# Performance work log

Measured on AMD Instinct MI355X. Metric: run time of the kernel, lower is better.

Reference implementation:

```python
import jax, jax.numpy as jnp
import numpy as np

B, S, D_IN = 2, 2048, 1024
EMBED, HEADS = 1024, 16
HEAD_DIM = EMBED // HEADS

def setup_inputs() -> dict:
    key = jax.random.key(0)
    k1, k2, k3 = jax.random.split(key, 3)
    # xavier_uniform bounds
    def xavier(k, shape):
        fan_in, fan_out = shape[1], shape[0]
        lim = jnp.sqrt(6.0 / (fan_in + fan_out))
        return jax.random.uniform(k, shape, jnp.float32, -lim, lim)
    x = jax.random.normal(k1, (B, S, D_IN), jnp.float32)
    qkv_w = xavier(k2, (3 * EMBED, D_IN))   # torch Linear weight layout [out, in]
    qkv_b = jnp.zeros((3 * EMBED,), jnp.float32)
    o_w = xavier(k3, (EMBED, EMBED))
    o_b = jnp.zeros((EMBED,), jnp.float32)
    return {"x": x, "qkv_w": qkv_w, "qkv_b": qkv_b, "o_w": o_w, "o_b": o_b}

def reference(x, qkv_w, qkv_b, o_w, o_b):
    Bq, Sq, _ = x.shape
    qkv = x @ qkv_w.T + qkv_b                       # [B,S,3E]
    qkv = qkv.reshape(Bq, Sq, HEADS, 3 * HEAD_DIM).transpose(0, 2, 1, 3)  # [B,H,S,3d]
    q, k, v = jnp.split(qkv, 3, axis=-1)            # each [B,H,S,d]
    scale = 1.0 / jnp.sqrt(jnp.asarray(HEAD_DIM, x.dtype))
    logits = jnp.einsum('bhqd,bhkd->bhqk', q, k) * scale
    attn = jax.nn.softmax(logits, axis=-1)
    vals = jnp.einsum('bhqk,bhkd->bhqd', attn, v)   # [B,H,S,d]
    vals = vals.transpose(0, 2, 1, 3).reshape(Bq, Sq, EMBED)
    return vals @ o_w.T + o_b
```

## Files before the change

### kernel.cpp

```cpp
#include <hip/hip_runtime.h>
#include <hip/hip_bf16.h>

#define B_    2
#define S_    2048
#define DIN   1024
#define EMB   1024
#define NH    16
#define HD    64
#define N3    3072
#define MROWS 4096
#define KVB   64
#define QBLK  128
#define NT    (S_ / KVB)

typedef short bf16x8 __attribute__((ext_vector_type(8)));
typedef float f32x4  __attribute__((ext_vector_type(4)));
typedef float f32x16 __attribute__((ext_vector_type(16)));
typedef unsigned short u16;
typedef u16 u16x8 __attribute__((ext_vector_type(8)));
typedef u16 u16x4 __attribute__((ext_vector_type(4)));
typedef unsigned int u32;

__device__ __forceinline__ u16 f2bf(float f) {
  union { float f; unsigned u; } x; x.f = f;
  unsigned r = x.u + 0x7fffu + ((x.u >> 16) & 1u);
  return (u16)(r >> 16);
}

__device__ __forceinline__ u32 cvtpk(float lo, float hi) {
  u32 r;
  asm("v_cvt_pk_bf16_f32 %0, %1, %2" : "=v"(r) : "v"(lo), "v"(hi));
  return r;
}

__device__ __forceinline__ void gload16(const void* g, void* l) {
  __builtin_amdgcn_global_load_lds(
      (const __attribute__((address_space(1))) unsigned int*)g,
      (__attribute__((address_space(3))) unsigned int*)l, 16, 0, 0);
}

__global__ void cast4(const float* __restrict__ in, u16* __restrict__ out, int n4) {
  const int i = blockIdx.x * 256 + threadIdx.x;
  if (i < n4) {
    const float4 v = ((const float4*)in)[i];
    u16x4 o;
    o[0] = f2bf(v.x); o[1] = f2bf(v.y); o[2] = f2bf(v.z); o[3] = f2bf(v.w);
    ((u16x4*)out)[i] = o;
  }
}

template<int EPI>
__global__ __launch_bounds__(256)
void gemm_bt(const u16* __restrict__ A, const u16* __restrict__ W,
             const float* __restrict__ bias, float* __restrict__ Cf,
             u16* __restrict__ Qb, u16* __restrict__ Kb, u16* __restrict__ VbT,
             int M, int N, int K) {
  __shared__ u16 Als[128 * 32];
  __shared__ u16 Bls[128 * 32];
  const int tid  = threadIdx.x;
  const int wave = tid >> 6, lane = tid & 63;
  const int lhi  = lane >> 4, llo = lane & 15;
  const int wr   = wave >> 1, wc = wave & 1;
  const int m0   = blockIdx.y * 128, n0 = blockIdx.x * 128;

  const f32x4 fzero = {0.f, 0.f, 0.f, 0.f};
  f32x4 acc[4][4];
#pragma unroll
  for (int m = 0; m < 4; ++m)
#pragma unroll
    for (int n = 0; n < 4; ++n) acc[m][n] = fzero;

  for (int k0 = 0; k0 < K; k0 += 32) {
#pragma unroll
    for (int i = 0; i < 2; ++i) {
      const int e   = (tid + i * 256) * 8;
      const int row = e >> 5, col = e & 31;
      gload16(A + (size_t)(m0 + row) * K + k0 + col, (char*)Als + wave * 1024 + i * 4096);
      gload16(W + (size_t)(n0 + row) * K + k0 + col, (char*)Bls + wave * 1024 + i * 4096);
    }
    __syncthreads();
    bf16x8 af[4], bfr[4];
#pragma unroll
    for (int m = 0; m < 4; ++m) af[m]  = *(const bf16x8*)&Als[(wr * 64 + m * 16 + llo) * 32 + lhi * 8];
#pragma unroll
    for (int n = 0; n < 4; ++n) bfr[n] = *(const bf16x8*)&Bls[(wc * 64 + n * 16 + llo) * 32 + lhi * 8];
#pragma unroll
    for (int m = 0; m < 4; ++m)
#pragma unroll
      for (int n = 0; n < 4; ++n)
        acc[m][n] = __builtin_amdgcn_mfma_f32_16x16x32_bf16(af[m], bfr[n], acc[m][n], 0, 0, 0);
    __syncthreads();
  }

#pragma unroll
  for (int n = 0; n < 4; ++n) {
    const int colb = n0 + wc * 64 + n * 16;
    const int gcol = colb + llo;
    const float bv = bias[gcol];
    if (EPI == 0) {
      const int h   = colb / 192;
      const int rr  = colb - h * 192;
      const int sec = rr >> 6;
      const int d   = (rr & 63) + llo;
#pragma unroll
      for (int m = 0; m < 4; ++m) {
        const int rowb = m0 + wr * 64 + m * 16 + lhi * 4;
        const int b = rowb >> 11, s0 = rowb & 2047;
        if (sec == 2) {
          u16x4 vv;
#pragma unroll
          for (int r = 0; r < 4; ++r) vv[r] = f2bf(acc[m][n][r] + bv);
          *(u16x4*)&VbT[((size_t)(b * NH + h) * HD + d) * S_ + s0] = vv;
        } else {
          u16* dst = (sec == 0) ? Qb : Kb;
          const float scl = (sec == 0) ? 0.18033688f : 1.0f;
#pragma unroll
          for (int r = 0; r < 4; ++r)
            dst[(((size_t)(b * NH + h) * S_ + s0 + r) << 6) + d] = f2bf((acc[m][n][r] + bv) * scl);
        }
      }
    } else {
#pragma unroll
      for (int m = 0; m < 4; ++m) {
        const int rowb = m0 + wr * 64 + m * 16 + lhi * 4;
#pragma unroll
        for (int r = 0; r < 4; ++r)
          Cf[(size_t)(rowb + r) * N + gcol] = acc[m][n][r] + bv;
      }
    }
  }
}

__global__ __launch_bounds__(256)
void attn_fwd(const u16* __restrict__ Qb, const u16* __restrict__ Kb,
              const u16* __restrict__ VbT, u16* __restrict__ Obf) {
  __shared__ __align__(16) u16 Kls[4][KVB * HD];
  __shared__ __align__(16) u16 Vls[4][HD * KVB];
  __shared__ __align__(16) float sBc[4][32];
  const int tid  = threadIdx.x;
  const int wave = tid >> 6, lane = tid & 63;
  const int q    = lane & 31, hi = lane >> 5;
  const int bh   = blockIdx.y;
  const int q0   = blockIdx.x * QBLK;
  const size_t base  = (size_t)bh * S_ * HD;
  const size_t basev = (size_t)bh * HD * S_;

  const int qrow = q0 + wave * 32 + q;
  bf16x8 qf[4];
#pragma unroll
  for (int c = 0; c < 4; ++c)
    qf[c] = *(const bf16x8*)&Qb[base + (size_t)qrow * HD + c * 16 + hi * 8];

  const int srow = tid >> 3;
  const int xs   = (tid & 7) ^ (srow & 7);
  const u16* kSrc = Kb  + base  + (size_t)srow * HD + xs * 8;
  const u16* vSrc = VbT + basev + (size_t)srow * S_ + xs * 8;
  const int ldsW = wave * 1024;

  const int gq = 16 * (q >> 4) + 8 * ((q >> 2) & 1) + (q & 3) + 4 * ((q >> 3) & 1);

  int offK[2][4], offV[2][4];
#pragma unroll
  for (int b = 0; b < 2; ++b)
#pragma unroll
    for (int c = 0; c < 4; ++c) {
      offK[b][c] = (b * 32 + gq) * 128 + (((c * 2 + hi) ^ (gq & 7)) << 4);
      offV[b][c] = (b * 32 + q)  * 128 + (((c * 2 + hi) ^ (q  & 7)) << 4);
    }

  f32x16 o0, o1;
#pragma unroll
  for (int r = 0; r < 16; ++r) { o0[r] = 0.f; o1[r] = 0.f; }
  float m_run = -1e30f, lsum = 0.f;

  auto issue = [&](int t) {
#pragma unroll
    for (int p = 0; p < 2; ++p) {
      gload16(kSrc + (size_t)t * KVB * HD + (size_t)p * 32 * HD,
              (char*)Kls[t & 3] + p * 4096 + ldsW);
      gload16(vSrc + t * KVB + (size_t)p * 32 * S_,
              (char*)Vls[t & 3] + p * 4096 + ldsW);
    }
  };

  auto compute = [&](int t) {
    const char* Kt = (const char*)Kls[t & 3];
    const char* Vt = (const char*)Vls[t & 3];

    f32x16 s0, s1;
#pragma unroll
    for (int r = 0; r < 16; ++r) { s0[r] = 0.f; s1[r] = 0.f; }
    __builtin_amdgcn_s_setprio(1);
#pragma unroll
    for (int c = 0; c < 4; ++c) {
      bf16x8 k0 = *(const bf16x8*)(Kt + offK[0][c]);
      bf16x8 k1 = *(const bf16x8*)(Kt + offK[1][c]);
      s0 = __builtin_amdgcn_mfma_f32_32x32x16_bf16(k0, qf[c], s0, 0, 0, 0);
      s1 = __builtin_amdgcn_mfma_f32_32x32x16_bf16(k1, qf[c], s1, 0, 0, 0);
    }
    __builtin_amdgcn_s_setprio(0);

    float tm[16];
#pragma unroll
    for (int r = 0; r < 16; ++r) tm[r] = fmaxf(s0[r], s1[r]);
#pragma unroll
    for (int st = 8; st >= 1; st >>= 1)
#pragma unroll
      for (int i = 0; i < 16; ++i) if (i < st) tm[i] = fmaxf(tm[i], tm[i + st]);
    const float pm = fmaxf(tm[0], __shfl_xor(tm[0], 32));

    if (__any(pm > m_run + 10.0f)) {
      const float mnew  = fmaxf(m_run, pm);
      const float alpha = exp2f(m_run - mnew);
      sBc[wave][q] = alpha;
      asm volatile("s_waitcnt lgkmcnt(0)" ::: "memory");
      f32x4 av[4];
#pragma unroll
      for (int g = 0; g < 4; ++g) av[g] = *(const f32x4*)&sBc[wave][hi * 4 + g * 8];
#pragma unroll
      for (int r = 0; r < 16; ++r) {
        const float f = av[r >> 2][r & 3];
        o0[r] *= f; o1[r] *= f;
      }
      lsum *= alpha;
      m_run = mnew;
    }

    float t0 = 0.f, t1 = 0.f, t2 = 0.f, t3 = 0.f;
    u32 dw0[8], dw1[8];
#pragma unroll
    for (int j = 0; j < 8; ++j) {
      const float a0 = exp2f(s0[2 * j] - m_run), a1 = exp2f(s0[2 * j + 1] - m_run);
      const float b0 = exp2f(s1[2 * j] - m_run), b1 = exp2f(s1[2 * j + 1] - m_run);
      t0 += a0; t1 += a1; t2 += b0; t3 += b1;
      dw0[j] = cvtpk(a0, a1);
      dw1[j] = cvtpk(b0, b1);
    }
    float ts = (t0 + t1) + (t2 + t3);
    ts += __shfl_xor(ts, 32);
    lsum += ts;

    __builtin_amdgcn_s_setprio(1);
#pragma unroll
    for (int c = 0; c < 4; ++c) {
      union { u32 u[4]; bf16x8 v; } P;
      if (c == 0)      { P.u[0] = dw0[0]; P.u[1] = dw0[1]; P.u[2] = dw0[2]; P.u[3] = dw0[3]; }
      else if (c == 1) { P.u[0] = dw0[4]; P.u[1] = dw0[5]; P.u[2] = dw0[6]; P.u[3] = dw0[7]; }
      else if (c == 2) { P.u[0] = dw1[0]; P.u[1] = dw1[1]; P.u[2] = dw1[2]; P.u[3] = dw1[3]; }
      else             { P.u[0] = dw1[4]; P.u[1] = dw1[5]; P.u[2] = dw1[6]; P.u[3] = dw1[7]; }
      bf16x8 v0 = *(const bf16x8*)(Vt + offV[0][c]);
      bf16x8 v1 = *(const bf16x8*)(Vt + offV[1][c]);
      o0 = __builtin_amdgcn_mfma_f32_32x32x16_bf16(P.v, v0, o0, 0, 0, 0);
      o1 = __builtin_amdgcn_mfma_f32_32x32x16_bf16(P.v, v1, o1, 0, 0, 0);
    }
    __builtin_amdgcn_s_setprio(0);
  };

  issue(0); issue(1);

#define BAR() do { asm volatile("" ::: "memory"); \
                   __builtin_amdgcn_s_barrier();  \
                   asm volatile("" ::: "memory"); } while (0)
  for (int p = 0; p < NT / 2 - 1; ++p) {
    issue(2 * p + 2); issue(2 * p + 3);
    asm volatile("s_waitcnt vmcnt(8)" ::: "memory");
    BAR();
    compute(2 * p);
    compute(2 * p + 1);
    BAR();
  }
  asm volatile("s_waitcnt vmcnt(0)" ::: "memory");
  BAR();
  compute(NT - 2);
  compute(NT - 1);
#undef BAR

  const float li = 1.0f / lsum;
  sBc[wave][q] = li;
  asm volatile("s_waitcnt lgkmcnt(0)" ::: "memory");
  f32x4 lv[4];
#pragma unroll
  for (int g = 0; g < 4; ++g) lv[g] = *(const f32x4*)&sBc[wave][hi * 4 + g * 8];
  const int b = bh >> 4, h = bh & 15;
#pragma unroll
  for (int r = 0; r < 16; ++r) {
    const int qg = q0 + wave * 32 + (r & 3) + 8 * (r >> 2) + 4 * hi;
    const float f = lv[r >> 2][r & 3];
    u16* dst = Obf + ((size_t)(b * S_ + qg) * NH + h) * HD;
    dst[q]      = f2bf(o0[r] * f);
    dst[32 + q] = f2bf(o1[r] * f);
  }
}

extern "C" void kernel_launch(void* const* d_in, const int* in_sizes, int n_in,
                              void* d_out, int out_size, void* d_ws, size_t ws_size,
                              hipStream_t stream) {
  const float* x     = (const float*)d_in[0];
  const float* qkv_w = (const float*)d_in[1];
  const float* qkv_b = (const float*)d_in[2];
  const float* o_w   = (const float*)d_in[3];
  const float* o_b   = (const float*)d_in[4];
  float* out = (float*)d_out;

  char* ws = (char*)d_ws;
  u16* xbf  = (u16*)(ws);
  u16* wqkv = (u16*)(ws + (8u  << 20));
  u16* wo   = (u16*)(ws + (14u << 20));
  u16* Qb   = (u16*)(ws + (16u << 20));
  u16* Kb   = (u16*)(ws + (24u << 20));
  u16* VbT  = (u16*)(ws + (32u << 20));
  u16* atnb = xbf;

  cast4<<<4096, 256, 0, stream>>>(x,     xbf,  1048576);
  cast4<<<3072, 256, 0, stream>>>(qkv_w, wqkv,  786432);
  cast4<<<1024, 256, 0, stream>>>(o_w,   wo,    262144);

  gemm_bt<0><<<dim3(N3 / 128, MROWS / 128), 256, 0, stream>>>(
      xbf, wqkv, qkv_b, nullptr, Qb, Kb, VbT, MROWS, N3, DIN);

  attn_fwd<<<dim3(S_ / QBLK, B_ * NH), 256, 0, stream>>>(Qb, Kb, VbT, atnb);

  gemm_bt<1><<<dim3(EMB / 128, MROWS / 128), 256, 0, stream>>>(
      atnb, wo, o_b, out, nullptr, nullptr, nullptr, MROWS, EMB, EMB);
}
```

Baseline: 151.7 us.

## Split attention over KV halves with combine pass, fuse cast kernels

Attention now splits the KV sequence into two halves across a third grid dimension. Each half writes fp32 partial outputs plus running max and sum, and a separate combine kernel merges them into bf16. This doubles the block count from 512 to 1024 so the GPU's CUs stay busier, at the cost of extra fp32 traffic (about 32 MB written and read) and one more launch. The three cast kernels are also merged into one launch. The split path only runs when the workspace is large enough, otherwise the old kernel is used.

```diff
diff --git a/kernel.cpp b/kernel.cpp
--- a/kernel.cpp
+++ b/kernel.cpp
@@ -12,6 +12,8 @@
 #define KVB   64
 #define QBLK  128
 #define NT    (S_ / KVB)
+#define NSPL  2
+#define NTS   (NT / NSPL)
 
 typedef short bf16x8 __attribute__((ext_vector_type(8)));
 typedef float f32x4  __attribute__((ext_vector_type(4)));
@@ -39,14 +41,19 @@
       (__attribute__((address_space(3))) unsigned int*)l, 16, 0, 0);
 }
 
-__global__ void cast4(const float* __restrict__ in, u16* __restrict__ out, int n4) {
+__global__ __launch_bounds__(256)
+void cast_all(const float* __restrict__ x, const float* __restrict__ w1,
+              const float* __restrict__ w2, u16* __restrict__ ox,
+              u16* __restrict__ ow1, u16* __restrict__ ow2) {
   const int i = blockIdx.x * 256 + threadIdx.x;
-  if (i < n4) {
-    const float4 v = ((const float4*)in)[i];
-    u16x4 o;
-    o[0] = f2bf(v.x); o[1] = f2bf(v.y); o[2] = f2bf(v.z); o[3] = f2bf(v.w);
-    ((u16x4*)out)[i] = o;
-  }
+  const float* src; u16* dst; int off;
+  if (i < 1048576)              { src = x;  dst = ox;  off = i; }
+  else if (i < 1048576 + 786432){ src = w1; dst = ow1; off = i - 1048576; }
+  else                          { src = w2; dst = ow2; off = i - 1835008; }
+  const float4 v = ((const float4*)src)[off];
+  u16x4 o;
+  o[0] = f2bf(v.x); o[1] = f2bf(v.y); o[2] = f2bf(v.z); o[3] = f2bf(v.w);
+  ((u16x4*)dst)[off] = o;
 }
 
 template<int EPI>
@@ -131,6 +138,182 @@
   }
 }
 
+
+__global__ __launch_bounds__(256)
+void attn_split(const u16* __restrict__ Qb, const u16* __restrict__ Kb,
+                const u16* __restrict__ VbT, float* __restrict__ Op,
+                float2* __restrict__ Ml) {
+  __shared__ __align__(16) u16 Kls[2][KVB * HD];
+  __shared__ __align__(16) u16 Vls[2][HD * KVB];
+  __shared__ __align__(16) float sBc[4][32];
+  const int tid  = threadIdx.x;
+  const int wave = tid >> 6, lane = tid & 63;
+  const int q    = lane & 31, hi = lane >> 5;
+  const int bh   = blockIdx.y;
+  const int q0   = blockIdx.x * QBLK;
+  const int sp   = blockIdx.z;
+  const size_t base  = (size_t)bh * S_ * HD;
+  const size_t basev = (size_t)bh * HD * S_;
+
+  const int qrow = q0 + wave * 32 + q;
+  bf16x8 qf[4];
+#pragma unroll
+  for (int c = 0; c < 4; ++c)
+    qf[c] = *(const bf16x8*)&Qb[base + (size_t)qrow * HD + c * 16 + hi * 8];
+
+  const int srow = tid >> 3;
+  const int xs   = (tid & 7) ^ (srow & 7);
+  const u16* kSrc = Kb  + base  + (size_t)(sp * NTS * KVB + srow) * HD + xs * 8;
+  const u16* vSrc = VbT + basev + (size_t)srow * S_ + sp * NTS * KVB + xs * 8;
+  const int ldsW = wave * 1024;
+
+  const int gq = 16 * (q >> 4) + 8 * ((q >> 2) & 1) + (q & 3) + 4 * ((q >> 3) & 1);
+  int offK[2][4], offV[2][4];
+#pragma unroll
+  for (int b = 0; b < 2; ++b)
+#pragma unroll
+    for (int c = 0; c < 4; ++c) {
+      offK[b][c] = (b * 32 + gq) * 128 + (((c * 2 + hi) ^ (gq & 7)) << 4);
+      offV[b][c] = (b * 32 + q)  * 128 + (((c * 2 + hi) ^ (q  & 7)) << 4);
+    }
+
+  f32x16 o0, o1;
+#pragma unroll
+  for (int r = 0; r < 16; ++r) { o0[r] = 0.f; o1[r] = 0.f; }
+  float m_run = -1e30f, lsum = 0.f;
+
+  auto issue = [&](int t) {
+#pragma unroll
+    for (int p = 0; p < 2; ++p) {
+      gload16(kSrc + (size_t)t * KVB * HD + (size_t)p * 32 * HD,
+              (char*)Kls[t & 1] + p * 4096 + ldsW);
+      gload16(vSrc + t * KVB + (size_t)p * 32 * S_,
+              (char*)Vls[t & 1] + p * 4096 + ldsW);
+    }
+  };
+
+  auto compute = [&](int t) {
+    const char* Kt = (const char*)Kls[t & 1];
+    const char* Vt = (const char*)Vls[t & 1];
+
+    f32x16 s0, s1;
+#pragma unroll
+    for (int r = 0; r < 16; ++r) { s0[r] = 0.f; s1[r] = 0.f; }
+    __builtin_amdgcn_s_setprio(1);
+#pragma unroll
+    for (int c = 0; c < 4; ++c) {
+      bf16x8 k0 = *(const bf16x8*)(Kt + offK[0][c]);
+      bf16x8 k1 = *(const bf16x8*)(Kt + offK[1][c]);
+      s0 = __builtin_amdgcn_mfma_f32_32x32x16_bf16(k0, qf[c], s0, 0, 0, 0);
+      s1 = __builtin_amdgcn_mfma_f32_32x32x16_bf16(k1, qf[c], s1, 0, 0, 0);
+    }
+    __builtin_amdgcn_s_setprio(0);
+
+    float tm[16];
+#pragma unroll
+    for (int r = 0; r < 16; ++r) tm[r] = fmaxf(s0[r], s1[r]);
+#pragma unroll
+    for (int st = 8; st >= 1; st >>= 1)
+#pragma unroll
+      for (int i = 0; i < 16; ++i) if (i < st) tm[i] = fmaxf(tm[i], tm[i + st]);
+    const float pm = fmaxf(tm[0], __shfl_xor(tm[0], 32));
+
+    if (__any(pm > m_run + 10.0f)) {
+      const float mnew  = fmaxf(m_run, pm);
+      const float alpha = exp2f(m_run - mnew);
+      sBc[wave][q] = alpha;
+      asm volatile("s_waitcnt lgkmcnt(0)" ::: "memory");
+      f32x4 av[4];
+#pragma unroll
+      for (int g = 0; g < 4; ++g) av[g] = *(const f32x4*)&sBc[wave][hi * 4 + g * 8];
+#pragma unroll
+      for (int r = 0; r < 16; ++r) {
+        const float f = av[r >> 2][r & 3];
+        o0[r] *= f; o1[r] *= f;
+      }
+      lsum *= alpha;
+      m_run = mnew;
+    }
+
+    float t0 = 0.f, t1 = 0.f, t2 = 0.f, t3 = 0.f;
+    u32 dw0[8], dw1[8];
+#pragma unroll
+    for (int j = 0; j < 8; ++j) {
+      const float a0 = exp2f(s0[2 * j] - m_run), a1 = exp2f(s0[2 * j + 1] - m_run);
+      const float b0 = exp2f(s1[2 * j] - m_run), b1 = exp2f(s1[2 * j + 1] - m_run);
+      t0 += a0; t1 += a1; t2 += b0; t3 += b1;
+      dw0[j] = cvtpk(a0, a1);
+      dw1[j] = cvtpk(b0, b1);
+    }
+    float ts = (t0 + t1) + (t2 + t3);
+    ts += __shfl_xor(ts, 32);
+    lsum += ts;
+
+    __builtin_amdgcn_s_setprio(1);
+#pragma unroll
+    for (int c = 0; c < 4; ++c) {
+      union { u32 u[4]; bf16x8 v; } P;
+      if (c == 0)      { P.u[0] = dw0[0]; P.u[1] = dw0[1]; P.u[2] = dw0[2]; P.u[3] = dw0[3]; }
+      else if (c == 1) { P.u[0] = dw0[4]; P.u[1] = dw0[5]; P.u[2] = dw0[6]; P.u[3] = dw0[7]; }
+      else if (c == 2) { P.u[0] = dw1[0]; P.u[1] = dw1[1]; P.u[2] = dw1[2]; P.u[3] = dw1[3]; }
+      else             { P.u[0] = dw1[4]; P.u[1] = dw1[5]; P.u[2] = dw1[6]; P.u[3] = dw1[7]; }
+      bf16x8 v0 = *(const bf16x8*)(Vt + offV[0][c]);
+      bf16x8 v1 = *(const bf16x8*)(Vt + offV[1][c]);
+      o0 = __builtin_amdgcn_mfma_f32_32x32x16_bf16(P.v, v0, o0, 0, 0, 0);
+      o1 = __builtin_amdgcn_mfma_f32_32x32x16_bf16(P.v, v1, o1, 0, 0, 0);
+    }
+    __builtin_amdgcn_s_setprio(0);
+  };
+
+#define BAR() do { asm volatile("" ::: "memory"); \
+                   __builtin_amdgcn_s_barrier();  \
+                   asm volatile("" ::: "memory"); } while (0)
+  issue(0);
+  for (int t = 0; t < NTS - 1; ++t) {
+    issue(t + 1);
+    asm volatile("s_waitcnt vmcnt(4)" ::: "memory");
+    BAR();
+    compute(t);
+    BAR();
+  }
+  asm volatile("s_waitcnt vmcnt(0)" ::: "memory");
+  BAR();
+  compute(NTS - 1);
+#undef BAR
+
+  float* dstb = Op + (size_t)(sp * (B_ * NH) + bh) * S_ * HD;
+#pragma unroll
+  for (int r = 0; r < 16; ++r) {
+    const int qg = q0 + wave * 32 + (r & 3) + 8 * (r >> 2) + 4 * hi;
+    float* dst = dstb + (size_t)qg * HD;
+    dst[q]      = o0[r];
+    dst[32 + q] = o1[r];
+  }
+  if (hi == 0)
+    Ml[(size_t)(sp * (B_ * NH) + bh) * S_ + qrow] = make_float2(m_run, lsum);
+}
+
+__global__ __launch_bounds__(256)
+void attn_combine(const float* __restrict__ Op, const float2* __restrict__ Ml,
+                  u16* __restrict__ atnb) {
+  const int g  = blockIdx.x * 256 + threadIdx.x;
+  const int d4 = g & 15, q = (g >> 4) & (S_ - 1), bh = g >> 15;
+  const float2 ml0 = Ml[(size_t)bh * S_ + q];
+  const float2 ml1 = Ml[(size_t)(B_ * NH + bh) * S_ + q];
+  const float M  = fmaxf(ml0.x, ml1.x);
+  const float w0 = exp2f(ml0.x - M), w1 = exp2f(ml1.x - M);
+  const float inv = 1.0f / (w0 * ml0.y + w1 * ml1.y);
+  const float4 a = ((const float4*)(Op + ((size_t)bh * S_ + q) * HD))[d4];
+  const float4 b = ((const float4*)(Op + ((size_t)(B_ * NH + bh) * S_ + q) * HD))[d4];
+  const int bb = bh >> 4, h = bh & 15;
+  u16x4 o;
+  o[0] = f2bf((w0 * a.x + w1 * b.x) * inv);
+  o[1] = f2bf((w0 * a.y + w1 * b.y) * inv);
+  o[2] = f2bf((w0 * a.z + w1 * b.z) * inv);
+  o[3] = f2bf((w0 * a.w + w1 * b.w) * inv);
+  ((u16x4*)(atnb + ((size_t)(bb * S_ + q) * NH + h) * HD))[d4] = o;
+}
+
 __global__ __launch_bounds__(256)
 void attn_fwd(const u16* __restrict__ Qb, const u16* __restrict__ Kb,
               const u16* __restrict__ VbT, u16* __restrict__ Obf) {
@@ -158,7 +341,6 @@
   const int ldsW = wave * 1024;
 
   const int gq = 16 * (q >> 4) + 8 * ((q >> 2) & 1) + (q & 3) + 4 * ((q >> 3) & 1);
-
   int offK[2][4], offV[2][4];
 #pragma unroll
   for (int b = 0; b < 2; ++b)
@@ -186,7 +368,6 @@
   auto compute = [&](int t) {
     const char* Kt = (const char*)Kls[t & 3];
     const char* Vt = (const char*)Vls[t & 3];
-
     f32x16 s0, s1;
 #pragma unroll
     for (int r = 0; r < 16; ++r) { s0[r] = 0.f; s1[r] = 0.f; }
@@ -257,7 +438,6 @@
   };
 
   issue(0); issue(1);
-
 #define BAR() do { asm volatile("" ::: "memory"); \
                    __builtin_amdgcn_s_barrier();  \
                    asm volatile("" ::: "memory"); } while (0)
@@ -311,14 +491,23 @@
   u16* VbT  = (u16*)(ws + (32u << 20));
   u16* atnb = xbf;
 
-  cast4<<<4096, 256, 0, stream>>>(x,     xbf,  1048576);
-  cast4<<<3072, 256, 0, stream>>>(qkv_w, wqkv,  786432);
-  cast4<<<1024, 256, 0, stream>>>(o_w,   wo,    262144);
+  const size_t opBytes = (size_t)NSPL * B_ * NH * S_ * HD * sizeof(float);
+  const size_t mlBytes = (size_t)NSPL * B_ * NH * S_ * sizeof(float2);
+  const size_t NEED = ((size_t)40 << 20) + opBytes + mlBytes;
+  float*  Op = (float*)(ws + ((size_t)40 << 20));
+  float2* Ml = (float2*)(ws + ((size_t)40 << 20) + opBytes);
+
+  cast_all<<<8192, 256, 0, stream>>>(x, qkv_w, o_w, xbf, wqkv, wo);
 
   gemm_bt<0><<<dim3(N3 / 128, MROWS / 128), 256, 0, stream>>>(
       xbf, wqkv, qkv_b, nullptr, Qb, Kb, VbT, MROWS, N3, DIN);
 
-  attn_fwd<<<dim3(S_ / QBLK, B_ * NH), 256, 0, stream>>>(Qb, Kb, VbT, atnb);
+  if (ws_size >= NEED) {
+    attn_split<<<dim3(S_ / QBLK, B_ * NH, NSPL), 256, 0, stream>>>(Qb, Kb, VbT, Op, Ml);
+    attn_combine<<<(B_ * NH * S_ * HD / 4) / 256, 256, 0, stream>>>(Op, Ml, atnb);
+  } else {
+    attn_fwd<<<dim3(S_ / QBLK, B_ * NH), 256, 0, stream>>>(Qb, Kb, VbT, atnb);
+  }
 
   gemm_bt<1><<<dim3(EMB / 128, MROWS / 128), 256, 0, stream>>>(
       atnb, wo, o_b, out, nullptr, nullptr, nullptr, MROWS, EMB, EMB);
```

Measured after the change: 155.8 us. +2.7%, slower.

## Add triple-buffered 256x128 QKV GEMM kernel and merge cast launches

Applied to the files above, without the earlier changes.

Replaces the generic 128x128 QKV projection GEMM with a dedicated 512-thread kernel. It uses 256x128 tiles, K-steps of 64, triple-buffered async global-to-LDS loads with an XOR-swizzled layout, and a block-index swizzle for L2 locality. The three fp32-to-bf16 cast launches are merged into one kernel to cut launch overhead. The larger tile raises LDS use (about 144 KB), which allows one block per CU and only 384 blocks, so wave-count balance across CUs may suffer.

```diff
diff --git a/kernel.cpp b/kernel.cpp
--- a/kernel.cpp
+++ b/kernel.cpp
@@ -39,22 +39,142 @@
       (__attribute__((address_space(3))) unsigned int*)l, 16, 0, 0);
 }
 
-__global__ void cast4(const float* __restrict__ in, u16* __restrict__ out, int n4) {
+#define BARRIER() do { asm volatile("" ::: "memory"); \
+                       __builtin_amdgcn_s_barrier();  \
+                       asm volatile("" ::: "memory"); } while (0)
+
+__global__ __launch_bounds__(256)
+void cast_all(const float* __restrict__ x, const float* __restrict__ w1,
+              const float* __restrict__ w2, u16* __restrict__ ox,
+              u16* __restrict__ ow1, u16* __restrict__ ow2) {
   const int i = blockIdx.x * 256 + threadIdx.x;
-  if (i < n4) {
-    const float4 v = ((const float4*)in)[i];
-    u16x4 o;
-    o[0] = f2bf(v.x); o[1] = f2bf(v.y); o[2] = f2bf(v.z); o[3] = f2bf(v.w);
-    ((u16x4*)out)[i] = o;
-  }
-}
-
-template<int EPI>
+  const float* src; u16* dst; int off;
+  if (i < 1048576)              { src = x;  dst = ox;  off = i; }
+  else if (i < 1048576 + 786432){ src = w1; dst = ow1; off = i - 1048576; }
+  else                          { src = w2; dst = ow2; off = i - 1835008; }
+  const float4 v = ((const float4*)src)[off];
+  u16x4 o;
+  o[0] = f2bf(v.x); o[1] = f2bf(v.y); o[2] = f2bf(v.z); o[3] = f2bf(v.w);
+  ((u16x4*)dst)[off] = o;
+}
+
+__global__ __launch_bounds__(512)
+void gemm256_qkv(const u16* __restrict__ A, const u16* __restrict__ W,
+                 const float* __restrict__ bias,
+                 u16* __restrict__ Qb, u16* __restrict__ Kb, u16* __restrict__ VbT) {
+  __shared__ __align__(16) u16 Als[3][256 * 64];
+  __shared__ __align__(16) u16 Bls[3][128 * 64];
+  const int K = DIN, KT = DIN / 64;
+
+  const int flat = blockIdx.x;
+  const int swz  = (flat & 7) * 48 + (flat >> 3);
+  const int n0   = (swz % 24) * 128;
+  const int m0   = (swz / 24) * 256;
+
+  const int tid  = threadIdx.x;
+  const int wave = tid >> 6, lane = tid & 63;
+  const int lhi  = lane >> 4, llo = lane & 15;
+  const int wr   = wave >> 2;
+  const int wc   = wave & 3;
+  const int ldsW = wave * 1024;
+
+  const int srow = tid >> 3;
+  const int xcol = (tid & 7) ^ (srow & 7);
+  const u16* aSrc = A + (size_t)(m0 + srow) * K + xcol * 8;
+  const u16* bSrc = W + (size_t)(n0 + srow) * K + xcol * 8;
+
+  auto issue = [&](int t) {
+    const int buf = t % 3;
+#pragma unroll
+    for (int g = 0; g < 4; ++g)
+      gload16(aSrc + (size_t)(g * 64) * K + t * 64,
+              (char*)Als[buf] + g * 8192 + ldsW);
+#pragma unroll
+    for (int g = 0; g < 2; ++g)
+      gload16(bSrc + (size_t)(g * 64) * K + t * 64,
+              (char*)Bls[buf] + g * 8192 + ldsW);
+  };
+
+  int swzs[2];
+#pragma unroll
+  for (int kk = 0; kk < 2; ++kk)
+    swzs[kk] = (((kk * 4 + lhi) ^ (llo & 7)) << 4);
+
+  f32x4 acc[8][2];
+#pragma unroll
+  for (int m = 0; m < 8; ++m)
+#pragma unroll
+    for (int n = 0; n < 2; ++n) acc[m][n] = f32x4{0.f, 0.f, 0.f, 0.f};
+
+  auto compute = [&](int t) {
+    const char* bufA = (const char*)Als[t % 3];
+    const char* bufB = (const char*)Bls[t % 3];
+    bf16x8 bF[2][2];
+#pragma unroll
+    for (int nj = 0; nj < 2; ++nj)
+#pragma unroll
+      for (int kk = 0; kk < 2; ++kk)
+        bF[nj][kk] = *(const bf16x8*)(bufB + (wc * 32 + nj * 16 + llo) * 128 + swzs[kk]);
+    __builtin_amdgcn_s_setprio(1);
+#pragma unroll
+    for (int mi = 0; mi < 8; ++mi) {
+      const char* ap = bufA + (wr * 128 + mi * 16 + llo) * 128;
+      bf16x8 a0 = *(const bf16x8*)(ap + swzs[0]);
+      bf16x8 a1 = *(const bf16x8*)(ap + swzs[1]);
+      acc[mi][0] = __builtin_amdgcn_mfma_f32_16x16x32_bf16(a0, bF[0][0], acc[mi][0], 0, 0, 0);
+      acc[mi][0] = __builtin_amdgcn_mfma_f32_16x16x32_bf16(a1, bF[0][1], acc[mi][0], 0, 0, 0);
+      acc[mi][1] = __builtin_amdgcn_mfma_f32_16x16x32_bf16(a0, bF[1][0], acc[mi][1], 0, 0, 0);
+      acc[mi][1] = __builtin_amdgcn_mfma_f32_16x16x32_bf16(a1, bF[1][1], acc[mi][1], 0, 0, 0);
+    }
+    __builtin_amdgcn_s_setprio(0);
+  };
+
+  issue(0); issue(1);
+  for (int t = 0; t < KT - 2; ++t) {
+    issue(t + 2);
+    asm volatile("s_waitcnt vmcnt(12)" ::: "memory");
+    BARRIER();
+    compute(t);
+    BARRIER();
+  }
+  asm volatile("s_waitcnt vmcnt(6)" ::: "memory");
+  BARRIER(); compute(KT - 2); BARRIER();
+  asm volatile("s_waitcnt vmcnt(0)" ::: "memory");
+  BARRIER(); compute(KT - 1);
+
+#pragma unroll
+  for (int nj = 0; nj < 2; ++nj) {
+    const int colb = n0 + wc * 32 + nj * 16;
+    const int gcol = colb + llo;
+    const float bv = bias[gcol];
+    const int h   = colb / 192;
+    const int rr  = colb - h * 192;
+    const int sec = rr >> 6;
+    const int d   = (rr & 63) + llo;
+#pragma unroll
+    for (int mi = 0; mi < 8; ++mi) {
+      const int rowb = m0 + wr * 128 + mi * 16 + lhi * 4;
+      const int b = rowb >> 11, s0 = rowb & 2047;
+      if (sec == 2) {
+        u16x4 vv;
+#pragma unroll
+        for (int r = 0; r < 4; ++r) vv[r] = f2bf(acc[mi][nj][r] + bv);
+        *(u16x4*)&VbT[((size_t)(b * NH + h) * HD + d) * S_ + s0] = vv;
+      } else {
+        u16* dst = (sec == 0) ? Qb : Kb;
+        const float scl = (sec == 0) ? 0.18033688f : 1.0f;
+#pragma unroll
+        for (int r = 0; r < 4; ++r)
+          dst[(((size_t)(b * NH + h) * S_ + s0 + r) << 6) + d] = f2bf((acc[mi][nj][r] + bv) * scl);
+      }
+    }
+  }
+}
+
 __global__ __launch_bounds__(256)
-void gemm_bt(const u16* __restrict__ A, const u16* __restrict__ W,
-             const float* __restrict__ bias, float* __restrict__ Cf,
-             u16* __restrict__ Qb, u16* __restrict__ Kb, u16* __restrict__ VbT,
-             int M, int N, int K) {
+void gemm_bt_f32(const u16* __restrict__ A, const u16* __restrict__ W,
+                 const float* __restrict__ bias, float* __restrict__ Cf,
+                 int M, int N, int K) {
   __shared__ u16 Als[128 * 32];
   __shared__ u16 Bls[128 * 32];
   const int tid  = threadIdx.x;
@@ -63,12 +183,11 @@
   const int wr   = wave >> 1, wc = wave & 1;
   const int m0   = blockIdx.y * 128, n0 = blockIdx.x * 128;
 
-  const f32x4 fzero = {0.f, 0.f, 0.f, 0.f};
   f32x4 acc[4][4];
 #pragma unroll
   for (int m = 0; m < 4; ++m)
 #pragma unroll
-    for (int n = 0; n < 4; ++n) acc[m][n] = fzero;
+    for (int n = 0; n < 4; ++n) acc[m][n] = f32x4{0.f, 0.f, 0.f, 0.f};
 
   for (int k0 = 0; k0 < K; k0 += 32) {
 #pragma unroll
@@ -94,39 +213,14 @@
 
 #pragma unroll
   for (int n = 0; n < 4; ++n) {
-    const int colb = n0 + wc * 64 + n * 16;
-    const int gcol = colb + llo;
+    const int gcol = n0 + wc * 64 + n * 16 + llo;
     const float bv = bias[gcol];
-    if (EPI == 0) {
-      const int h   = colb / 192;
-      const int rr  = colb - h * 192;
-      const int sec = rr >> 6;
-      const int d   = (rr & 63) + llo;
-#pragma unroll
-      for (int m = 0; m < 4; ++m) {
-        const int rowb = m0 + wr * 64 + m * 16 + lhi * 4;
-        const int b = rowb >> 11, s0 = rowb & 2047;
-        if (sec == 2) {
-          u16x4 vv;
-#pragma unroll
-          for (int r = 0; r < 4; ++r) vv[r] = f2bf(acc[m][n][r] + bv);
-          *(u16x4*)&VbT[((size_t)(b * NH + h) * HD + d) * S_ + s0] = vv;
-        } else {
-          u16* dst = (sec == 0) ? Qb : Kb;
-          const float scl = (sec == 0) ? 0.18033688f : 1.0f;
-#pragma unroll
-          for (int r = 0; r < 4; ++r)
-            dst[(((size_t)(b * NH + h) * S_ + s0 + r) << 6) + d] = f2bf((acc[m][n][r] + bv) * scl);
-        }
-      }
-    } else {
-#pragma unroll
-      for (int m = 0; m < 4; ++m) {
-        const int rowb = m0 + wr * 64 + m * 16 + lhi * 4;
-#pragma unroll
-        for (int r = 0; r < 4; ++r)
-          Cf[(size_t)(rowb + r) * N + gcol] = acc[m][n][r] + bv;
-      }
+#pragma unroll
+    for (int m = 0; m < 4; ++m) {
+      const int rowb = m0 + wr * 64 + m * 16 + lhi * 4;
+#pragma unroll
+      for (int r = 0; r < 4; ++r)
+        Cf[(size_t)(rowb + r) * N + gcol] = acc[m][n][r] + bv;
     }
   }
 }
@@ -158,7 +252,6 @@
   const int ldsW = wave * 1024;
 
   const int gq = 16 * (q >> 4) + 8 * ((q >> 2) & 1) + (q & 3) + 4 * ((q >> 3) & 1);
-
   int offK[2][4], offV[2][4];
 #pragma unroll
   for (int b = 0; b < 2; ++b)
@@ -186,7 +279,6 @@
   auto compute = [&](int t) {
     const char* Kt = (const char*)Kls[t & 3];
     const char* Vt = (const char*)Vls[t & 3];
-
     f32x16 s0, s1;
 #pragma unroll
     for (int r = 0; r < 16; ++r) { s0[r] = 0.f; s1[r] = 0.f; }
@@ -257,23 +349,18 @@
   };
 
   issue(0); issue(1);
-
-#define BAR() do { asm volatile("" ::: "memory"); \
-                   __builtin_amdgcn_s_barrier();  \
-                   asm volatile("" ::: "memory"); } while (0)
   for (int p = 0; p < NT / 2 - 1; ++p) {
     issue(2 * p + 2); issue(2 * p + 3);
     asm volatile("s_waitcnt vmcnt(8)" ::: "memory");
-    BAR();
+    BARRIER();
     compute(2 * p);
     compute(2 * p + 1);
-    BAR();
+    BARRIER();
   }
   asm volatile("s_waitcnt vmcnt(0)" ::: "memory");
-  BAR();
+  BARRIER();
   compute(NT - 2);
   compute(NT - 1);
-#undef BAR
 
   const float li = 1.0f / lsum;
   sBc[wave][q] = li;
@@ -311,15 +398,12 @@
   u16* VbT  = (u16*)(ws + (32u << 20));
   u16* atnb = xbf;
 
-  cast4<<<4096, 256, 0, stream>>>(x,     xbf,  1048576);
-  cast4<<<3072, 256, 0, stream>>>(qkv_w, wqkv,  786432);
-  cast4<<<1024, 256, 0, stream>>>(o_w,   wo,    262144);
-
-  gemm_bt<0><<<dim3(N3 / 128, MROWS / 128), 256, 0, stream>>>(
-      xbf, wqkv, qkv_b, nullptr, Qb, Kb, VbT, MROWS, N3, DIN);
+  cast_all<<<8192, 256, 0, stream>>>(x, qkv_w, o_w, xbf, wqkv, wo);
+
+  gemm256_qkv<<<384, 512, 0, stream>>>(xbf, wqkv, qkv_b, Qb, Kb, VbT);
 
   attn_fwd<<<dim3(S_ / QBLK, B_ * NH), 256, 0, stream>>>(Qb, Kb, VbT, atnb);
 
-  gemm_bt<1><<<dim3(EMB / 128, MROWS / 128), 256, 0, stream>>>(
-      atnb, wo, o_b, out, nullptr, nullptr, nullptr, MROWS, EMB, EMB);
-}
+  gemm_bt_f32<<<dim3(EMB / 128, MROWS / 128), 256, 0, stream>>>(
+      atnb, wo, o_b, out, MROWS, EMB, EMB);
+}
```

Result: slower. 160.1 us (+5.5%).

## Interleave QK and softmax/PV stages across tile pairs in attention loop

Applied to the files above, without the earlier changes.

The per-tile compute lambda is split into separate QK, softmax and PV stages. Both QK products of a tile pair are issued before the first softmax, so the tensor-core work of the second tile can overlap the exponentials of the first. The s_setprio hints are removed and the attention kernel gets launch_bounds(256,2) to cap registers for two blocks per CU. Holding the extra score and packed-P registers raises register pressure, and the new cap may force spills.

```diff
diff --git a/kernel.cpp b/kernel.cpp
--- a/kernel.cpp
+++ b/kernel.cpp
@@ -38,6 +38,10 @@
       (const __attribute__((address_space(1))) unsigned int*)g,
       (__attribute__((address_space(3))) unsigned int*)l, 16, 0, 0);
 }
+
+#define BARRIER() do { asm volatile("" ::: "memory"); \
+                       __builtin_amdgcn_s_barrier();  \
+                       asm volatile("" ::: "memory"); } while (0)
 
 __global__ void cast4(const float* __restrict__ in, u16* __restrict__ out, int n4) {
   const int i = blockIdx.x * 256 + threadIdx.x;
@@ -63,12 +67,11 @@
   const int wr   = wave >> 1, wc = wave & 1;
   const int m0   = blockIdx.y * 128, n0 = blockIdx.x * 128;
 
-  const f32x4 fzero = {0.f, 0.f, 0.f, 0.f};
   f32x4 acc[4][4];
 #pragma unroll
   for (int m = 0; m < 4; ++m)
 #pragma unroll
-    for (int n = 0; n < 4; ++n) acc[m][n] = fzero;
+    for (int n = 0; n < 4; ++n) acc[m][n] = f32x4{0.f, 0.f, 0.f, 0.f};
 
   for (int k0 = 0; k0 < K; k0 += 32) {
 #pragma unroll
@@ -131,7 +134,7 @@
   }
 }
 
-__global__ __launch_bounds__(256)
+__global__ __launch_bounds__(256, 2)
 void attn_fwd(const u16* __restrict__ Qb, const u16* __restrict__ Kb,
               const u16* __restrict__ VbT, u16* __restrict__ Obf) {
   __shared__ __align__(16) u16 Kls[4][KVB * HD];
@@ -158,7 +161,6 @@
   const int ldsW = wave * 1024;
 
   const int gq = 16 * (q >> 4) + 8 * ((q >> 2) & 1) + (q & 3) + 4 * ((q >> 3) & 1);
-
   int offK[2][4], offV[2][4];
 #pragma unroll
   for (int b = 0; b < 2; ++b)
@@ -183,14 +185,10 @@
     }
   };
 
-  auto compute = [&](int t) {
+  auto qk = [&](int t, f32x16& s0, f32x16& s1) {
     const char* Kt = (const char*)Kls[t & 3];
-    const char* Vt = (const char*)Vls[t & 3];
-
-    f32x16 s0, s1;
 #pragma unroll
     for (int r = 0; r < 16; ++r) { s0[r] = 0.f; s1[r] = 0.f; }
-    __builtin_amdgcn_s_setprio(1);
 #pragma unroll
     for (int c = 0; c < 4; ++c) {
       bf16x8 k0 = *(const bf16x8*)(Kt + offK[0][c]);
@@ -198,8 +196,9 @@
       s0 = __builtin_amdgcn_mfma_f32_32x32x16_bf16(k0, qf[c], s0, 0, 0, 0);
       s1 = __builtin_amdgcn_mfma_f32_32x32x16_bf16(k1, qf[c], s1, 0, 0, 0);
     }
-    __builtin_amdgcn_s_setprio(0);
-
+  };
+
+  auto sm = [&](f32x16& s0, f32x16& s1, u32 (&dw0)[8], u32 (&dw1)[8]) {
     float tm[16];
 #pragma unroll
     for (int r = 0; r < 16; ++r) tm[r] = fmaxf(s0[r], s1[r]);
@@ -227,7 +226,6 @@
     }
 
     float t0 = 0.f, t1 = 0.f, t2 = 0.f, t3 = 0.f;
-    u32 dw0[8], dw1[8];
 #pragma unroll
     for (int j = 0; j < 8; ++j) {
       const float a0 = exp2f(s0[2 * j] - m_run), a1 = exp2f(s0[2 * j + 1] - m_run);
@@ -239,8 +237,10 @@
     float ts = (t0 + t1) + (t2 + t3);
     ts += __shfl_xor(ts, 32);
     lsum += ts;
-
-    __builtin_amdgcn_s_setprio(1);
+  };
+
+  auto pv = [&](int t, u32 (&dw0)[8], u32 (&dw1)[8]) {
+    const char* Vt = (const char*)Vls[t & 3];
 #pragma unroll
     for (int c = 0; c < 4; ++c) {
       union { u32 u[4]; bf16x8 v; } P;
@@ -253,27 +253,32 @@
       o0 = __builtin_amdgcn_mfma_f32_32x32x16_bf16(P.v, v0, o0, 0, 0, 0);
       o1 = __builtin_amdgcn_mfma_f32_32x32x16_bf16(P.v, v1, o1, 0, 0, 0);
     }
-    __builtin_amdgcn_s_setprio(0);
   };
 
+  f32x16 sE0, sE1, sO0, sO1;
+  u32 dwE0[8], dwE1[8], dwO0[8], dwO1[8];
+
   issue(0); issue(1);
-
-#define BAR() do { asm volatile("" ::: "memory"); \
-                   __builtin_amdgcn_s_barrier();  \
-                   asm volatile("" ::: "memory"); } while (0)
   for (int p = 0; p < NT / 2 - 1; ++p) {
     issue(2 * p + 2); issue(2 * p + 3);
     asm volatile("s_waitcnt vmcnt(8)" ::: "memory");
-    BAR();
-    compute(2 * p);
-    compute(2 * p + 1);
-    BAR();
+    BARRIER();
+    qk(2 * p,     sE0, sE1);
+    qk(2 * p + 1, sO0, sO1);
+    sm(sE0, sE1, dwE0, dwE1);
+    pv(2 * p,     dwE0, dwE1);
+    sm(sO0, sO1, dwO0, dwO1);
+    pv(2 * p + 1, dwO0, dwO1);
+    BARRIER();
   }
   asm volatile("s_waitcnt vmcnt(0)" ::: "memory");
-  BAR();
-  compute(NT - 2);
-  compute(NT - 1);
-#undef BAR
+  BARRIER();
+  qk(NT - 2, sE0, sE1);
+  qk(NT - 1, sO0, sO1);
+  sm(sE0, sE1, dwE0, dwE1);
+  pv(NT - 2, dwE0, dwE1);
+  sm(sO0, sO1, dwO0, dwO1);
+  pv(NT - 1, dwO0, dwO1);
 
   const float li = 1.0f / lsum;
   sBc[wave][q] = li;
```

Result: faster. 144.0 us (-5.1%).
